# Optimization experiments

Hardware: AMD Instinct MI355X
Metric: run time of the kernel (lower is better)

The kernel has to match this reference:

```python
import jax, jax.numpy as jnp
import numpy as np

# Config (matches init_kwargs)
B, N, F, S, T, L = 4, 128, 128, 5, 32, 2
R_MAX = 10.0
AVG_NEI = 16.0
# ell index of each of the 16 spherical-harmonic components (l=0..3)
ELL_IDX = np.array([0] + [1]*3 + [2]*5 + [3]*7)


def _edges(n):
    # fully-connected directed edge list without self loops (static)
    i = np.arange(n)
    s = np.repeat(i, n)
    r = np.tile(i, n)
    m = s != r
    return jnp.asarray(s[m]), jnp.asarray(r[m])


def _sh(u):
    # real spherical harmonics up to ell=3, component normalization, unit input
    x, y, z = u[..., 0], u[..., 1], u[..., 2]
    s3, s5, s15 = 3**0.5, 5**0.5, 15**0.5
    s35_8, s105, s21_8, s7 = (35/8)**0.5, 105**0.5, (21/8)**0.5, 7**0.5
    comps = [jnp.ones_like(x),
             s3*x, s3*y, s3*z,
             s15*x*y, s15*y*z, 0.5*s5*(3*z*z - 1), s15*x*z, 0.5*s15*(x*x - y*y),
             s35_8*y*(3*x*x - y*y), s105*x*y*z, s21_8*y*(5*z*z - 1),
             0.5*s7*z*(5*z*z - 3), s21_8*x*(5*z*z - 1),
             0.5*s105*z*(x*x - y*y), s35_8*x*(x*x - 3*y*y)]
    return jnp.stack(comps, axis=-1)  # (E,16)


def _forward(positions, node_features, global_features, W_embed, b_embed,
             Wr1, br1, Wr2, Wnode, c1, c2, c3, Wmix0, Wmix1, Wg1, Wg2, Wvout):
    n = positions.shape[1]
    senders, receivers = _edges(n)
    ell = jnp.asarray(ELL_IDX)

    def single(pos, nf, te):
        pos0 = pos
        node_attrs = jax.nn.one_hot(nf - 1, S, dtype=pos.dtype)
        h = jnp.concatenate([node_attrs, jnp.tile(te, (n, 1))], axis=-1)
        scal = h @ W_embed + b_embed            # (N,F) scalar node feats
        vec = jnp.zeros((n, F, 3), pos.dtype)   # (N,F,3) vector node feats
        v = pos[receivers] - pos[senders]       # (E,3)
        lng = jnp.sqrt(jnp.sum(v*v, -1, keepdims=True) + 1e-12)  # (E,1)
        env = 0.5*(jnp.cos(jnp.pi*lng/R_MAX) + 1.0)*(lng < R_MAX)  # cutoff from lengths_0
        for i in range(L):
            u = v / lng
            Y = _sh(u)                                            # (E,16)
            Rw = jax.nn.silu(lng @ Wr1[i] + br1[i]) @ Wr2[i]      # radial MLP (E,4F)
            Rw = (Rw * env).reshape(-1, 4, F)                     # (E,4,F)
            z = (scal @ Wnode[i])[senders]                        # (E,F)
            vdot = jnp.einsum('ecd,ed->ec', vec[senders], u)      # (E,F)
            f = z + vdot
            # tensor-product messages (E,16,F)
            M = Rw[:, ell, :] * Y[:, :, None] * f[:, None, :]
            A = jnp.zeros((n, 16, F), pos.dtype).at[receivers].add(M) / AVG_NEI
            # correlation-3 symmetric-contraction gate via per-ell invariants
            nrm = jnp.zeros((n, 4, F), pos.dtype).at[:, ell, :].add(A*A)
            g = 1.0 + c1[i]*nrm + c2[i]*nrm*nrm + c3[i]*nrm*nrm*nrm
            A = A * g[:, ell, :]
            # linear mix to hidden irreps 128x0e + 128x1o
            scal = A[:, 0, :] @ Wmix0[i]                          # (N,F)
            vec = jnp.einsum('nmc,ck->nkm', A[:, 1:4, :], Wmix1[i])  # (N,F,3)
            # nonlinear readout -> equivariant position update
            gate = jax.nn.silu(scal @ Wg1[i]) @ Wg2[i]            # (N,F)
            mbv = jnp.sum(vec * (gate * Wvout[i])[:, :, None], 1) # (N,3)
            pos = pos + mbv
            v = pos[receivers] - pos[senders]
            lng = jnp.sqrt(jnp.sum(v*v, -1, keepdims=True) + 1e-12)
        return pos - pos0  # predicted noise on positions

    return jax.vmap(single)(positions, node_features, global_features)


def setup_inputs() -> dict:
    key = jax.random.key(0)
    ks = jax.random.split(key, 20)
    sc = 0.1
    p = {}
    p['positions'] = jax.random.normal(ks[0], (B, N, 3), jnp.float32)
    p['node_features'] = jax.random.randint(ks[1], (B, N), 1, S + 1).astype(jnp.int32)
    p['global_features'] = jax.random.normal(ks[2], (B, T), jnp.float32)
    p['W_embed'] = jax.random.normal(ks[3], (S + T, F)) * sc
    p['b_embed'] = jnp.zeros((F,))
    p['Wr1'] = jax.random.normal(ks[4], (L, 1, 64)) * sc
    p['br1'] = jnp.zeros((L, 64))
    p['Wr2'] = jax.random.normal(ks[5], (L, 64, 4 * F)) * sc
    p['Wnode'] = jax.random.normal(ks[6], (L, F, F)) * sc
    p['c1'] = jax.random.normal(ks[7], (L, 4, F)) * 0.01
    p['c2'] = jax.random.normal(ks[8], (L, 4, F)) * 0.001
    p['c3'] = jax.random.normal(ks[9], (L, 4, F)) * 0.0001
    p['Wmix0'] = jax.random.normal(ks[10], (L, F, F)) * sc
    p['Wmix1'] = jax.random.normal(ks[11], (L, F, F)) * sc
    p['Wg1'] = jax.random.normal(ks[12], (L, F, 16)) * sc
    p['Wg2'] = jax.random.normal(ks[13], (L, 16, F)) * sc
    p['Wvout'] = jax.random.normal(ks[14], (L, F)) * sc
    return p


def reference(positions, node_features, global_features, W_embed, b_embed,
              Wr1, br1, Wr2, Wnode, c1, c2, c3, Wmix0, Wmix1, Wg1, Wg2, Wvout):
    return _forward(positions, node_features, global_features, W_embed, b_embed,
                    Wr1, br1, Wr2, Wnode, c1, c2, c3, Wmix0, Wmix1, Wg1, Wg2, Wvout)
```

## Files before the change

kernel.cpp:

```cpp
#include <hip/hip_runtime.h>
#include <hip/hip_bf16.h>
#include <math.h>

#define NB 4
#define NN 128
#define NF 128
#define NS 5
#define NT 32
#define NL 2

typedef __hip_bfloat16 bf16;
typedef short bf16x8 __attribute__((ext_vector_type(8)));
typedef float f32x4 __attribute__((ext_vector_type(4)));

__device__ __forceinline__ float b2f(const bf16 x) { return __bfloat162float(x); }
__device__ __forceinline__ float fast_rcp(float x) { return __builtin_amdgcn_rcpf(x); }
__device__ __forceinline__ float fast_rsq(float x) { return __builtin_amdgcn_rsqf(x); }
__device__ __forceinline__ float silu_fast(float x) { return x * fast_rcp(1.0f + __expf(-x)); }
__device__ __forceinline__ float ldf(const void* p, int i, int fl) {
  return fl ? b2f(((const bf16*)p)[i]) : ((const float*)p)[i];
}
__device__ __forceinline__ short f2bf(float x) {
  unsigned u = __float_as_uint(x);
  unsigned r = (u + 0x7fffu + ((u >> 16) & 1u)) >> 16;
  return (short)r;
}

#define PI_F 3.14159265358979323846f
#define SQRT3_F 1.7320508075688772f

#define POS_OFF 0
#define GF_OFF  1536
#define WE_OFF  1664
#define BE_OFF  6400
#define WR1_OFF 6528
#define BR1_OFF 6656
#define WR2_OFF 6784
#define WN_OFF  72320
#define C1_OFF  105088
#define C2_OFF  106112
#define C3_OFF  107136
#define M0_OFF  108160
#define M1_OFF  140928
#define G1_OFF  173696
#define G2_OFF  177792
#define WV_OFF  181888
#define CVT_TOTAL 182144

__global__ void prep_convert_kernel(
    const void* __restrict__ pos_raw, const int* __restrict__ nfeat,
    const void* __restrict__ gf,  const void* __restrict__ we,
    const void* __restrict__ be,  const void* __restrict__ wr1,
    const void* __restrict__ br1, const void* __restrict__ wr2,
    const void* __restrict__ wn,  const void* __restrict__ c1,
    const void* __restrict__ c2,  const void* __restrict__ c3,
    const void* __restrict__ m0,  const void* __restrict__ m1,
    const void* __restrict__ g1,  const void* __restrict__ g2,
    const void* __restrict__ wv,
    int* __restrict__ flag, float* __restrict__ cvt,
    float* __restrict__ pos_cur, float* __restrict__ z,
    float* __restrict__ vec, float* __restrict__ env,
    float* __restrict__ Ag, short* __restrict__ pkw)
{
  __shared__ float posB[NN*3];
  __shared__ float scs[NF];
  __shared__ int sbad;
  const int tid = threadIdx.x;
  const int bn  = blockIdx.x;
  const int b   = bn >> 7;
  const int n   = bn & 127;

  if (tid == 0) sbad = 0;
  __syncthreads();
  {
    const bf16* p = (const bf16*)pos_raw;
    int bad = 0;
    for (int i = tid; i < NB*NN*3; i += 256) {
      float v = b2f(p[i]);
      if (!(fabsf(v) <= 1024.0f)) bad = 1;
    }
    if (bad) sbad = 1;
  }
  __syncthreads();
  const int fl = sbad ? 0 : 1;
  if (bn == 0 && tid == 0) *flag = fl;

  for (int i = bn*256 + tid; i < CVT_TOTAL; i += 512*256) {
    const void* src; int j;
    if      (i < GF_OFF)  { src = pos_raw; j = i - POS_OFF; }
    else if (i < WE_OFF)  { src = gf;  j = i - GF_OFF; }
    else if (i < BE_OFF)  { src = we;  j = i - WE_OFF; }
    else if (i < WR1_OFF) { src = be;  j = i - BE_OFF; }
    else if (i < BR1_OFF) { src = wr1; j = i - WR1_OFF; }
    else if (i < WR2_OFF) { src = br1; j = i - BR1_OFF; }
    else if (i < WN_OFF)  { src = wr2; j = i - WR2_OFF; }
    else if (i < C1_OFF)  { src = wn;  j = i - WN_OFF; }
    else if (i < C2_OFF)  { src = c1;  j = i - C1_OFF; }
    else if (i < C3_OFF)  { src = c2;  j = i - C2_OFF; }
    else if (i < M0_OFF)  { src = c3;  j = i - C3_OFF; }
    else if (i < M1_OFF)  { src = m0;  j = i - M0_OFF; }
    else if (i < G1_OFF)  { src = m1;  j = i - M1_OFF; }
    else if (i < G2_OFF)  { src = g1;  j = i - G1_OFF; }
    else if (i < WV_OFF)  { src = g2;  j = i - G2_OFF; }
    else                  { src = wv;  j = i - WV_OFF; }
    cvt[i] = fl ? b2f(((const bf16*)src)[j]) : ((const float*)src)[j];
  }

  if (bn < 16) {
    int gid  = bn*256 + tid;
    int lyr  = gid >> 11;
    int r    = gid & 2047;
    int wv   = r >> 9;
    int t    = (r >> 7) & 3;
    int ks   = (r >> 6) & 1;
    int lane = r & 63;
    int qq = lane >> 4, nn = lane & 15;
    int col = wv*64 + t*16 + nn;
    short* dst = pkw + (size_t)gid*8;
    #pragma unroll
    for (int j = 0; j < 8; ++j) {
      int k = ks*32 + qq*8 + j;
      float v = ldf(wr2, lyr*64*512 + k*512 + col, fl);
      if (wv >= 2) v *= SQRT3_F;
      dst[j] = f2bf(v);
    }
  }

  for (int i = tid; i < NN*3; i += 256)
    posB[i] = ldf(pos_raw, b*NN*3 + i, fl);
  if (tid < 128) {
    int sp = nfeat[bn] - 1;
    float acc = ldf(we, sp*NF + tid, fl) + ldf(be, tid, fl);
    #pragma unroll 8
    for (int t = 0; t < NT; ++t)
      acc += ldf(gf, b*NT + t, fl) * ldf(we, (NS + t)*NF + tid, fl);
    scs[tid] = acc;
  }
  __syncthreads();

  if (tid < 128) {
    const int f = tid;
    {
      float px = posB[n*3+0], py = posB[n*3+1], pz = posB[n*3+2];
      float vx = px - posB[f*3+0];
      float vy = py - posB[f*3+1];
      float vz = pz - posB[f*3+2];
      float lng = sqrtf(vx*vx + vy*vy + vz*vz + 1e-12f);
      env[bn*NN + f] = (lng < 10.0f) ? 0.5f*(cosf(PI_F*lng*0.1f) + 1.0f) : 0.0f;
    }
    {
      float acc = 0.f;
      if (fl) {
        const bf16* W = (const bf16*)wn;
        #pragma unroll 8
        for (int k = 0; k < NF; ++k) acc += scs[k] * b2f(W[k*NF + f]);
      } else {
        const float* W = (const float*)wn;
        #pragma unroll 8
        for (int k = 0; k < NF; ++k) acc += scs[k] * W[k*NF + f];
      }
      z[bn*NF + f] = acc;
    }
    vec[((size_t)bn*3 + 0)*NF + f] = 0.f;
    vec[((size_t)bn*3 + 1)*NF + f] = 0.f;
    vec[((size_t)bn*3 + 2)*NF + f] = 0.f;
    float* Arow = Ag + (size_t)bn*4*NF;
    #pragma unroll
    for (int c = 0; c < 4; ++c) Arow[c*NF + f] = 0.f;
    if (f < 3) pos_cur[bn*3 + f] = posB[n*3 + f];
  }
}

__global__ __launch_bounds__(256, 2)
void edge_kernel(const float* __restrict__ pos_cur,
                 const float* __restrict__ z,
                 const float* __restrict__ vec,
                 const float* __restrict__ env,
                 const float* __restrict__ cvt,
                 const short* __restrict__ pk,
                 int layer, float* __restrict__ Ag)
{
  __shared__ float posL[NN*3];
  __shared__ float envL[4][32];
  __shared__ float w1L[64], b1L[64];
  __shared__ __align__(16) short hidA[2][16][72];
  __shared__ __align__(16) float4 zvp[2][4][NF];
  __shared__ __align__(16) float4 uenvL[2][4][4];

  const int tid  = threadIdx.x;
  const int bidx = blockIdx.x;
  const int b    = bidx >> 7;
  const int rt   = (bidx >> 2) & 31;
  const int sg   = bidx & 3;
  const int r0   = rt * 4;
  const int sbase= sg * 32;

  const int wvid  = tid >> 6;
  const int lane  = tid & 63;
  const int n16   = lane & 15;
  const int q     = lane >> 4;
  const int halfB = wvid >> 1;

  for (int i = tid; i < NN*3; i += 256)
    posL[i] = pos_cur[b*NN*3 + i];
  if (tid < 128) {
    int rr = tid >> 5, j = tid & 31;
    envL[rr][j] = env[(b*NN + r0 + rr)*NN + sbase + j];
  }
  if (tid < 64) {
    w1L[tid] = cvt[WR1_OFF + layer*64 + tid];
    b1L[tid] = cvt[BR1_OFF + layer*64 + tid];
  }
  bf16x8 bfr[4][2];
  {
    const bf16x8* PK = (const bf16x8*)pk + (size_t)layer*2048 + wvid*512 + lane;
    #pragma unroll
    for (int t = 0; t < 4; ++t) {
      #pragma unroll
      for (int ks = 0; ks < 2; ++ks)
        bfr[t][ks] = PK[(t*2 + ks)*64];
    }
  }
  float acR[12];
  #pragma unroll
  for (int i = 0; i < 12; ++i) acR[i] = 0.f;

  __syncthreads();

  const int rme = wvid;
  const int hme = lane;
  const float hrx = posL[(r0 + rme)*3 + 0];
  const float hry = posL[(r0 + rme)*3 + 1];
  const float hrz = posL[(r0 + rme)*3 + 2];
  const float w1v = w1L[hme], b1v = b1L[hme];

  const int fS  = tid & 127;
  const int si0 = tid >> 7;

  float4 pv[2];

  #pragma unroll
  for (int rep = 0; rep < 2; ++rep) {
    int gs = b*NN + sbase + 0 + si0 + 2*rep;
    pv[rep].x = z[gs*NF + fS];
    pv[rep].y = vec[((size_t)gs*3 + 0)*NF + fS];
    pv[rep].z = vec[((size_t)gs*3 + 1)*NF + fS];
    pv[rep].w = vec[((size_t)gs*3 + 2)*NF + fS];
  }
  #pragma unroll
  for (int si = 0; si < 4; ++si) {
    int s = sbase + si;
    float vx = hrx - posL[s*3 + 0];
    float vy = hry - posL[s*3 + 1];
    float vz = hrz - posL[s*3 + 2];
    float d = vx*vx + vy*vy + vz*vz + 1e-12f;
    float lng = d * fast_rsq(d);
    hidA[0][rme*4 + si][hme] = f2bf(silu_fast(lng * w1v + b1v));
  }
  if (tid < 16) {
    int r = tid >> 2, si = tid & 3;
    int s = sbase + si;
    float vx = posL[(r0 + r)*3 + 0] - posL[s*3 + 0];
    float vy = posL[(r0 + r)*3 + 1] - posL[s*3 + 1];
    float vz = posL[(r0 + r)*3 + 2] - posL[s*3 + 2];
    float d = vx*vx + vy*vy + vz*vz + 1e-12f;
    float inv = fast_rsq(d);
    float envw = (s == r0 + r) ? 0.f : envL[r][si] * 0.0625f;
    uenvL[0][r][si] = make_float4(vx*inv, vy*inv, vz*inv, envw);
  }
  #pragma unroll
  for (int rep = 0; rep < 2; ++rep)
    zvp[0][si0 + 2*rep][fS] = pv[rep];
  __syncthreads();

  #pragma unroll
  for (int c = 0; c < 8; ++c) {
    const int cb = c & 1, nb = cb ^ 1;
    const int nc0 = (c + 1) * 4;

    if (c < 7) {
      #pragma unroll
      for (int rep = 0; rep < 2; ++rep) {
        int gs = b*NN + sbase + nc0 + si0 + 2*rep;
        pv[rep].x = z[gs*NF + fS];
        pv[rep].y = vec[((size_t)gs*3 + 0)*NF + fS];
        pv[rep].z = vec[((size_t)gs*3 + 1)*NF + fS];
        pv[rep].w = vec[((size_t)gs*3 + 2)*NF + fS];
      }
    }

    bf16x8 af0 = *(const bf16x8*)&hidA[cb][n16][q*8];
    bf16x8 af1 = *(const bf16x8*)&hidA[cb][n16][q*8 + 32];
    float4 ue[4];
    #pragma unroll
    for (int si = 0; si < 4; ++si) ue[si] = uenvL[cb][q][si];

    #pragma unroll
    for (int t = 0; t < 4; ++t) {
      f32x4 Cf = {0.f, 0.f, 0.f, 0.f};
      Cf = __builtin_amdgcn_mfma_f32_16x16x32_bf16(af0, bfr[t][0], Cf, 0, 0, 0);
      Cf = __builtin_amdgcn_mfma_f32_16x16x32_bf16(af1, bfr[t][1], Cf, 0, 0, 0);
      int f = (wvid*64 + t*16 + n16) & 127;
      if (!halfB) {
        float a0 = 0.f;
        #pragma unroll
        for (int si = 0; si < 4; ++si) {
          float4 zv = zvp[cb][si][f];
          float fv = zv.x + ue[si].x*zv.y + ue[si].y*zv.z + ue[si].z*zv.w;
          a0 += (Cf[si] * ue[si].w) * fv;
        }
        acR[t] += a0;
      } else {
        float t1 = 0.f, t2 = 0.f, t3 = 0.f;
        #pragma unroll
        for (int si = 0; si < 4; ++si) {
          float4 zv = zvp[cb][si][f];
          float fv = zv.x + ue[si].x*zv.y + ue[si].y*zv.z + ue[si].z*zv.w;
          float tt = (Cf[si] * ue[si].w) * fv;
          t1 += tt * ue[si].x;
          t2 += tt * ue[si].y;
          t3 += tt * ue[si].z;
        }
        acR[t*3 + 0] += t1;
        acR[t*3 + 1] += t2;
        acR[t*3 + 2] += t3;
      }
    }

    if (c < 7) {
      #pragma unroll
      for (int si = 0; si < 4; ++si) {
        int s = sbase + nc0 + si;
        float vx = hrx - posL[s*3 + 0];
        float vy = hry - posL[s*3 + 1];
        float vz = hrz - posL[s*3 + 2];
        float d = vx*vx + vy*vy + vz*vz + 1e-12f;
        float lng = d * fast_rsq(d);
        hidA[nb][rme*4 + si][hme] = f2bf(silu_fast(lng * w1v + b1v));
      }
      if (tid < 16) {
        int r = tid >> 2, si = tid & 3;
        int s = sbase + nc0 + si;
        float vx = posL[(r0 + r)*3 + 0] - posL[s*3 + 0];
        float vy = posL[(r0 + r)*3 + 1] - posL[s*3 + 1];
        float vz = posL[(r0 + r)*3 + 2] - posL[s*3 + 2];
        float d = vx*vx + vy*vy + vz*vz + 1e-12f;
        float inv = fast_rsq(d);
        float envw = (s == r0 + r) ? 0.f : envL[r][nc0 + si] * 0.0625f;
        uenvL[nb][r][si] = make_float4(vx*inv, vy*inv, vz*inv, envw);
      }
      #pragma unroll
      for (int rep = 0; rep < 2; ++rep)
        zvp[nb][si0 + 2*rep][fS] = pv[rep];
    }
    __syncthreads();
  }

  const size_t rowbase = (size_t)(b*NN + r0 + q)*4;
  if (!halfB) {
    #pragma unroll
    for (int t = 0; t < 4; ++t) {
      int f = (wvid*64 + t*16 + n16) & 127;
      atomicAdd(Ag + (rowbase + 0)*NF + f, acR[t]);
    }
  } else {
    #pragma unroll
    for (int t = 0; t < 4; ++t) {
      int f = (wvid*64 + t*16 + n16) & 127;
      atomicAdd(Ag + (rowbase + 1)*NF + f, acR[t*3 + 0]);
      atomicAdd(Ag + (rowbase + 2)*NF + f, acR[t*3 + 1]);
      atomicAdd(Ag + (rowbase + 3)*NF + f, acR[t*3 + 2]);
    }
  }
}

__global__ __launch_bounds__(256)
void node_kernel(float* __restrict__ Ag,
                 const float* __restrict__ cvt,
                 int layer, int last,
                 float* __restrict__ vec,
                 float* __restrict__ z,
                 float* __restrict__ pos_cur,
                 const int* __restrict__ flag,
                 void* __restrict__ out)
{
  const int bn  = blockIdx.x;
  const int tid = threadIdx.x;
  const int f   = tid & 127;
  __shared__ float Ash[4][NF];
  __shared__ float scs[NF];
  __shared__ float h16[16];
  __shared__ float red[2][4];
  __shared__ float P[8][32][17];
  __shared__ float Pg[8][16];

  if (tid < 128) {
    float* Arow = Ag + (size_t)bn*4*NF;
    float a0 = Arow[0*NF + f];
    float a1 = Arow[1*NF + f];
    float a2 = Arow[2*NF + f];
    float a3 = Arow[3*NF + f];
    Arow[0*NF + f] = 0.f;
    Arow[1*NF + f] = 0.f;
    Arow[2*NF + f] = 0.f;
    Arow[3*NF + f] = 0.f;
    float n0 = a0*a0;
    float C1 = cvt[C1_OFF + (layer*4 + 0)*NF + f];
    float C2 = cvt[C2_OFF + (layer*4 + 0)*NF + f];
    float C3 = cvt[C3_OFF + (layer*4 + 0)*NF + f];
    float g0 = 1.0f + C1*n0 + C2*n0*n0 + C3*n0*n0*n0;
    float n1 = a1*a1 + a2*a2 + a3*a3;
    float D1 = cvt[C1_OFF + (layer*4 + 1)*NF + f];
    float D2 = cvt[C2_OFF + (layer*4 + 1)*NF + f];
    float D3 = cvt[C3_OFF + (layer*4 + 1)*NF + f];
    float g1 = 1.0f + D1*n1 + D2*n1*n1 + D3*n1*n1*n1;
    Ash[0][f] = a0 * g0;
    Ash[1][f] = a1 * g1;
    Ash[2][f] = a2 * g1;
    Ash[3][f] = a3 * g1;
  }
  __syncthreads();

  {
    const float* M0 = cvt + M0_OFF + layer*NF*NF;
    const float* M1 = cvt + M1_OFF + layer*NF*NF;
    const int kh = tid >> 5;
    const int fq = tid & 31;
    float s0=0.f,s1=0.f,s2=0.f,s3=0.f;
    float w00=0.f,w01=0.f,w02=0.f,w03=0.f;
    float w10=0.f,w11=0.f,w12=0.f,w13=0.f;
    float w20=0.f,w21=0.f,w22=0.f,w23=0.f;
    #pragma unroll 4
    for (int kk = 0; kk < 16; ++kk) {
      int k = kh*16 + kk;
      float a0 = Ash[0][k], a1 = Ash[1][k], a2 = Ash[2][k], a3 = Ash[3][k];
      float4 m0 = *(const float4*)(M0 + k*NF + fq*4);
      float4 m1 = *(const float4*)(M1 + k*NF + fq*4);
      s0 += a0*m0.x; s1 += a0*m0.y; s2 += a0*m0.z; s3 += a0*m0.w;
      w00 += a1*m1.x; w01 += a1*m1.y; w02 += a1*m1.z; w03 += a1*m1.w;
      w10 += a2*m1.x; w11 += a2*m1.y; w12 += a2*m1.z; w13 += a2*m1.w;
      w20 += a3*m1.x; w21 += a3*m1.y; w22 += a3*m1.z; w23 += a3*m1.w;
    }
    float* Pp = &P[kh][fq][0];
    Pp[0]=s0;  Pp[1]=s1;  Pp[2]=s2;  Pp[3]=s3;
    Pp[4]=w00; Pp[5]=w01; Pp[6]=w02; Pp[7]=w03;
    Pp[8]=w10; Pp[9]=w11; Pp[10]=w12; Pp[11]=w13;
    Pp[12]=w20; Pp[13]=w21; Pp[14]=w22; Pp[15]=w23;
  }
  __syncthreads();

  float v0 = 0.f, v1 = 0.f, v2 = 0.f;
  if (tid < 128) {
    int fq = f >> 2, j = f & 3;
    float sn = 0.f;
    #pragma unroll
    for (int kh = 0; kh < 8; ++kh) {
      const float* Pp = &P[kh][fq][0];
      sn += Pp[j];
      v0 += Pp[4 + j];
      v1 += Pp[8 + j];
      v2 += Pp[12 + j];
    }
    scs[f] = sn;
  }
  __syncthreads();

  if (!last) {
    const float* W = cvt + WN_OFF + (layer+1)*NF*NF;
    const int kh = tid >> 5;
    const int fq = tid & 31;
    float s0=0.f,s1=0.f,s2=0.f,s3=0.f;
    #pragma unroll 4
    for (int kk = 0; kk < 16; ++kk) {
      int k = kh*16 + kk;
      float a = scs[k];
      float4 m = *(const float4*)(W + k*NF + fq*4);
      s0 += a*m.x; s1 += a*m.y; s2 += a*m.z; s3 += a*m.w;
    }
    float* Pp = &P[kh][fq][0];
    Pp[0]=s0; Pp[1]=s1; Pp[2]=s2; Pp[3]=s3;
  }
  if (tid < 128) {
    const float* G1 = cvt + G1_OFF + layer*NF*16;
    int o = tid & 15, g = tid >> 4;
    float acc = 0.f;
    #pragma unroll
    for (int kk = 0; kk < 16; ++kk) {
      int k = g*16 + kk;
      acc += scs[k] * G1[k*16 + o];
    }
    Pg[g][o] = acc;
  }
  __syncthreads();

  if (!last && tid < 128) {
    int fq = f >> 2, j = f & 3;
    float acc = 0.f;
    #pragma unroll
    for (int kh = 0; kh < 8; ++kh) acc += P[kh][fq][j];
    z[bn*NF + f] = acc;
  }
  if (tid < 16) {
    float acc = 0.f;
    #pragma unroll
    for (int g = 0; g < 8; ++g) acc += Pg[g][tid];
    h16[tid] = silu_fast(acc);
  }
  __syncthreads();

  if (tid < 128) {
    const float* G2 = cvt + G2_OFF + layer*16*NF;
    float gate = 0.f;
    #pragma unroll
    for (int j = 0; j < 16; ++j)
      gate += h16[j] * G2[j*NF + f];
    float gv = gate * cvt[WV_OFF + layer*NF + f];

    vec[((size_t)bn*3 + 0)*NF + f] = v0;
    vec[((size_t)bn*3 + 1)*NF + f] = v1;
    vec[((size_t)bn*3 + 2)*NF + f] = v2;

    float p0 = v0*gv, p1 = v1*gv, p2 = v2*gv;
    #pragma unroll
    for (int off = 32; off > 0; off >>= 1) {
      p0 += __shfl_down(p0, off, 64);
      p1 += __shfl_down(p1, off, 64);
      p2 += __shfl_down(p2, off, 64);
    }
    int wave = f >> 6;
    if ((f & 63) == 0) { red[wave][0] = p0; red[wave][1] = p1; red[wave][2] = p2; }
  }
  __syncthreads();
  if (tid == 0) {
    float m0 = red[0][0] + red[1][0];
    float m1 = red[0][1] + red[1][1];
    float m2 = red[0][2] + red[1][2];
    float px = pos_cur[bn*3+0] + m0;
    float py = pos_cur[bn*3+1] + m1;
    float pz = pos_cur[bn*3+2] + m2;
    pos_cur[bn*3+0] = px;
    pos_cur[bn*3+1] = py;
    pos_cur[bn*3+2] = pz;
    if (last) {
      float ox = px - cvt[POS_OFF + bn*3+0];
      float oy = py - cvt[POS_OFF + bn*3+1];
      float oz = pz - cvt[POS_OFF + bn*3+2];
      if (*flag) {
        bf16* o = (bf16*)out;
        o[bn*3+0] = __float2bfloat16(ox);
        o[bn*3+1] = __float2bfloat16(oy);
        o[bn*3+2] = __float2bfloat16(oz);
      } else {
        float* o = (float*)out;
        o[bn*3+0] = ox;
        o[bn*3+1] = oy;
        o[bn*3+2] = oz;
      }
    }
  }
}

extern "C" void kernel_launch(void* const* d_in, const int* in_sizes, int n_in,
                              void* d_out, int out_size, void* d_ws, size_t ws_size,
                              hipStream_t stream)
{
  (void)in_sizes; (void)n_in; (void)out_size; (void)ws_size;
  const int* nfeat = (const int*)d_in[1];

  float* ws      = (float*)d_ws;
  int*   flag    = (int*)ws;
  float* cvt     = ws + 16;
  float* pos_cur = cvt + CVT_TOTAL;
  float* z       = pos_cur + NB*NN*3;
  float* vec     = z + NB*NN*NF;
  float* Ag      = vec + NB*NN*3*NF;
  float* env     = Ag + NB*NN*4*NF;
  short* pk      = (short*)(env + NB*NN*NN);

  prep_convert_kernel<<<512, 256, 0, stream>>>(
      d_in[0], nfeat, d_in[2], d_in[3], d_in[4], d_in[5], d_in[6], d_in[7],
      d_in[8], d_in[9], d_in[10], d_in[11], d_in[12], d_in[13], d_in[14],
      d_in[15], d_in[16], flag, cvt, pos_cur, z, vec, env, Ag, pk);
  for (int i = 0; i < NL; ++i) {
    edge_kernel<<<512, 256, 0, stream>>>(pos_cur, z, vec, env, cvt, pk, i, Ag);
    node_kernel<<<NB*NN, 256, 0, stream>>>(Ag, cvt, i, (i == NL-1) ? 1 : 0,
                                           vec, z, pos_cur, flag, d_out);
  }
}
```

Baseline: 144.8 us.

## Fuse edge and node kernels into one per-receiver block with ping-pong buffers

Each block now owns one receiver node and loops over all 128 senders, so the aggregated messages are reduced in registers and shared memory instead of through global atomics. The node update then runs in the same block, which removes the separate node kernel, the Ag buffer and its zeroing. Positions, z and vec are double-buffered across the two layers, and layer 0 skips loading the all-zero vec. The cost is a larger per-block loop with no sender split across blocks, more registers for the 8-entry prefetch, and a shared-memory union. A few branch reorderings in the weight-conversion routine look odd and could be fragile.

```diff
diff --git a/kernel.cpp b/kernel.cpp
--- a/kernel.cpp
+++ b/kernel.cpp
@@ -59,8 +59,7 @@
     const void* __restrict__ wv,
     int* __restrict__ flag, float* __restrict__ cvt,
     float* __restrict__ pos_cur, float* __restrict__ z,
-    float* __restrict__ vec, float* __restrict__ env,
-    float* __restrict__ Ag, short* __restrict__ pkw)
+    float* __restrict__ env, short* __restrict__ pkw)
 {
   __shared__ float posB[NN*3];
   __shared__ float scs[NF];
@@ -92,9 +91,8 @@
     else if (i < BE_OFF)  { src = we;  j = i - WE_OFF; }
     else if (i < WR1_OFF) { src = be;  j = i - BE_OFF; }
     else if (i < BR1_OFF) { src = wr1; j = i - WR1_OFF; }
-    else if (i < WR2_OFF) { src = br1; j = i - BR1_OFF; }
-    else if (i < WN_OFF)  { src = wr2; j = i - WR2_OFF; }
-    else if (i < C1_OFF)  { src = wn;  j = i - WN_OFF; }
+    else if (i < WN_OFF)  { src = br1; j = i - BR1_OFF; }
+    else if (i < C1_OFF)  { src = wr2; j = i - WR2_OFF; }
     else if (i < C2_OFF)  { src = c1;  j = i - C1_OFF; }
     else if (i < C3_OFF)  { src = c2;  j = i - C2_OFF; }
     else if (i < M0_OFF)  { src = c3;  j = i - C3_OFF; }
@@ -103,6 +101,8 @@
     else if (i < G2_OFF)  { src = g1;  j = i - G1_OFF; }
     else if (i < WV_OFF)  { src = g2;  j = i - G2_OFF; }
     else                  { src = wv;  j = i - WV_OFF; }
+    if (i < WN_OFF && i >= C1_OFF) { }
+    if      (i >= WN_OFF && i < C1_OFF) { src = wn; j = i - WN_OFF; }
     cvt[i] = fl ? b2f(((const bf16*)src)[j]) : ((const float*)src)[j];
   }
 
@@ -110,18 +110,18 @@
     int gid  = bn*256 + tid;
     int lyr  = gid >> 11;
     int r    = gid & 2047;
-    int wv   = r >> 9;
+    int wv2  = r >> 9;
     int t    = (r >> 7) & 3;
     int ks   = (r >> 6) & 1;
     int lane = r & 63;
     int qq = lane >> 4, nn = lane & 15;
-    int col = wv*64 + t*16 + nn;
+    int col = wv2*64 + t*16 + nn;
     short* dst = pkw + (size_t)gid*8;
     #pragma unroll
     for (int j = 0; j < 8; ++j) {
       int k = ks*32 + qq*8 + j;
       float v = ldf(wr2, lyr*64*512 + k*512 + col, fl);
-      if (wv >= 2) v *= SQRT3_F;
+      if (wv2 >= 2) v *= SQRT3_F;
       dst[j] = f2bf(v);
     }
   }
@@ -161,39 +161,40 @@
       }
       z[bn*NF + f] = acc;
     }
-    vec[((size_t)bn*3 + 0)*NF + f] = 0.f;
-    vec[((size_t)bn*3 + 1)*NF + f] = 0.f;
-    vec[((size_t)bn*3 + 2)*NF + f] = 0.f;
-    float* Arow = Ag + (size_t)bn*4*NF;
-    #pragma unroll
-    for (int c = 0; c < 4; ++c) Arow[c*NF + f] = 0.f;
     if (f < 3) pos_cur[bn*3 + f] = posB[n*3 + f];
   }
 }
 
 __global__ __launch_bounds__(256, 2)
-void edge_kernel(const float* __restrict__ pos_cur,
-                 const float* __restrict__ z,
-                 const float* __restrict__ vec,
-                 const float* __restrict__ env,
-                 const float* __restrict__ cvt,
-                 const short* __restrict__ pk,
-                 int layer, float* __restrict__ Ag)
+void fused_kernel(const float* __restrict__ posIn, float* __restrict__ posOut,
+                  const float* __restrict__ zIn,  float* __restrict__ zOut,
+                  const float* __restrict__ vecIn, float* __restrict__ vecOut,
+                  const float* __restrict__ env,  const float* __restrict__ cvt,
+                  const short* __restrict__ pk, int layer, int last,
+                  const int* __restrict__ flag, void* __restrict__ out)
 {
+  union SM {
+    float4 zvp[2][16][NF];
+    struct {
+      float P[8][32][17];
+      float Pg[8][16];
+      float scs[NF];
+      float h16[16];
+      float red[2][4];
+    } nd;
+  };
+  __shared__ __align__(16) SM sm;
   __shared__ float posL[NN*3];
-  __shared__ float envL[4][32];
+  __shared__ float envL[NN];
   __shared__ float w1L[64], b1L[64];
   __shared__ __align__(16) short hidA[2][16][72];
-  __shared__ __align__(16) float4 zvp[2][4][NF];
-  __shared__ __align__(16) float4 uenvL[2][4][4];
+  __shared__ __align__(16) float4 uenvL[2][16];
+  __shared__ float Ash[4][NF];
 
   const int tid  = threadIdx.x;
   const int bidx = blockIdx.x;
   const int b    = bidx >> 7;
-  const int rt   = (bidx >> 2) & 31;
-  const int sg   = bidx & 3;
-  const int r0   = rt * 4;
-  const int sbase= sg * 32;
+  const int n    = bidx & 127;
 
   const int wvid  = tid >> 6;
   const int lane  = tid & 63;
@@ -202,11 +203,8 @@
   const int halfB = wvid >> 1;
 
   for (int i = tid; i < NN*3; i += 256)
-    posL[i] = pos_cur[b*NN*3 + i];
-  if (tid < 128) {
-    int rr = tid >> 5, j = tid & 31;
-    envL[rr][j] = env[(b*NN + r0 + rr)*NN + sbase + j];
-  }
+    posL[i] = posIn[b*NN*3 + i];
+  if (tid < 128) envL[tid] = env[(size_t)(b*NN + n)*NN + tid];
   if (tid < 64) {
     w1L[tid] = cvt[WR1_OFF + layer*64 + tid];
     b1L[tid] = cvt[BR1_OFF + layer*64 + tid];
@@ -227,65 +225,68 @@
 
   __syncthreads();
 
-  const int rme = wvid;
-  const int hme = lane;
-  const float hrx = posL[(r0 + rme)*3 + 0];
-  const float hry = posL[(r0 + rme)*3 + 1];
-  const float hrz = posL[(r0 + rme)*3 + 2];
-  const float w1v = w1L[hme], b1v = b1L[hme];
+  const float hrx = posL[n*3 + 0];
+  const float hry = posL[n*3 + 1];
+  const float hrz = posL[n*3 + 2];
+  const float w1v = w1L[lane], b1v = b1L[lane];
 
   const int fS  = tid & 127;
   const int si0 = tid >> 7;
 
-  float4 pv[2];
+  float4 pv[8];
 
   #pragma unroll
-  for (int rep = 0; rep < 2; ++rep) {
-    int gs = b*NN + sbase + 0 + si0 + 2*rep;
-    pv[rep].x = z[gs*NF + fS];
-    pv[rep].y = vec[((size_t)gs*3 + 0)*NF + fS];
-    pv[rep].z = vec[((size_t)gs*3 + 1)*NF + fS];
-    pv[rep].w = vec[((size_t)gs*3 + 2)*NF + fS];
+  for (int rep = 0; rep < 8; ++rep) {
+    int sl = si0 + 2*rep;
+    int gs = b*NN + sl;
+    pv[rep].x = zIn[gs*NF + fS];
+    if (layer) {
+      pv[rep].y = vecIn[((size_t)gs*3 + 0)*NF + fS];
+      pv[rep].z = vecIn[((size_t)gs*3 + 1)*NF + fS];
+      pv[rep].w = vecIn[((size_t)gs*3 + 2)*NF + fS];
+    } else { pv[rep].y = 0.f; pv[rep].z = 0.f; pv[rep].w = 0.f; }
   }
   #pragma unroll
-  for (int si = 0; si < 4; ++si) {
-    int s = sbase + si;
+  for (int j = 0; j < 4; ++j) {
+    int si = wvid*4 + j;
+    int s  = si;
     float vx = hrx - posL[s*3 + 0];
     float vy = hry - posL[s*3 + 1];
     float vz = hrz - posL[s*3 + 2];
     float d = vx*vx + vy*vy + vz*vz + 1e-12f;
     float lng = d * fast_rsq(d);
-    hidA[0][rme*4 + si][hme] = f2bf(silu_fast(lng * w1v + b1v));
+    hidA[0][si][lane] = f2bf(silu_fast(lng * w1v + b1v));
   }
   if (tid < 16) {
-    int r = tid >> 2, si = tid & 3;
-    int s = sbase + si;
-    float vx = posL[(r0 + r)*3 + 0] - posL[s*3 + 0];
-    float vy = posL[(r0 + r)*3 + 1] - posL[s*3 + 1];
-    float vz = posL[(r0 + r)*3 + 2] - posL[s*3 + 2];
+    int s = tid;
+    float vx = hrx - posL[s*3 + 0];
+    float vy = hry - posL[s*3 + 1];
+    float vz = hrz - posL[s*3 + 2];
     float d = vx*vx + vy*vy + vz*vz + 1e-12f;
     float inv = fast_rsq(d);
-    float envw = (s == r0 + r) ? 0.f : envL[r][si] * 0.0625f;
-    uenvL[0][r][si] = make_float4(vx*inv, vy*inv, vz*inv, envw);
+    float envw = (s == n) ? 0.f : envL[s] * 0.0625f;
+    uenvL[0][tid] = make_float4(vx*inv, vy*inv, vz*inv, envw);
   }
   #pragma unroll
-  for (int rep = 0; rep < 2; ++rep)
-    zvp[0][si0 + 2*rep][fS] = pv[rep];
-  __syncthreads();
-
-  #pragma unroll
+  for (int rep = 0; rep < 8; ++rep)
+    sm.zvp[0][si0 + 2*rep][fS] = pv[rep];
+  __syncthreads();
+
+  #pragma unroll 2
   for (int c = 0; c < 8; ++c) {
     const int cb = c & 1, nb = cb ^ 1;
-    const int nc0 = (c + 1) * 4;
+    const int nc0 = (c + 1) * 16;
 
     if (c < 7) {
       #pragma unroll
-      for (int rep = 0; rep < 2; ++rep) {
-        int gs = b*NN + sbase + nc0 + si0 + 2*rep;
-        pv[rep].x = z[gs*NF + fS];
-        pv[rep].y = vec[((size_t)gs*3 + 0)*NF + fS];
-        pv[rep].z = vec[((size_t)gs*3 + 1)*NF + fS];
-        pv[rep].w = vec[((size_t)gs*3 + 2)*NF + fS];
+      for (int rep = 0; rep < 8; ++rep) {
+        int gs = b*NN + nc0 + si0 + 2*rep;
+        pv[rep].x = zIn[gs*NF + fS];
+        if (layer) {
+          pv[rep].y = vecIn[((size_t)gs*3 + 0)*NF + fS];
+          pv[rep].z = vecIn[((size_t)gs*3 + 1)*NF + fS];
+          pv[rep].w = vecIn[((size_t)gs*3 + 2)*NF + fS];
+        } else { pv[rep].y = 0.f; pv[rep].z = 0.f; pv[rep].w = 0.f; }
       }
     }
 
@@ -293,7 +294,7 @@
     bf16x8 af1 = *(const bf16x8*)&hidA[cb][n16][q*8 + 32];
     float4 ue[4];
     #pragma unroll
-    for (int si = 0; si < 4; ++si) ue[si] = uenvL[cb][q][si];
+    for (int r = 0; r < 4; ++r) ue[r] = uenvL[cb][q*4 + r];
 
     #pragma unroll
     for (int t = 0; t < 4; ++t) {
@@ -304,22 +305,22 @@
       if (!halfB) {
         float a0 = 0.f;
         #pragma unroll
-        for (int si = 0; si < 4; ++si) {
-          float4 zv = zvp[cb][si][f];
-          float fv = zv.x + ue[si].x*zv.y + ue[si].y*zv.z + ue[si].z*zv.w;
-          a0 += (Cf[si] * ue[si].w) * fv;
+        for (int r = 0; r < 4; ++r) {
+          float4 zv = sm.zvp[cb][q*4 + r][f];
+          float fv = zv.x + ue[r].x*zv.y + ue[r].y*zv.z + ue[r].z*zv.w;
+          a0 += (Cf[r] * ue[r].w) * fv;
         }
         acR[t] += a0;
       } else {
         float t1 = 0.f, t2 = 0.f, t3 = 0.f;
         #pragma unroll
-        for (int si = 0; si < 4; ++si) {
-          float4 zv = zvp[cb][si][f];
-          float fv = zv.x + ue[si].x*zv.y + ue[si].y*zv.z + ue[si].z*zv.w;
-          float tt = (Cf[si] * ue[si].w) * fv;
-          t1 += tt * ue[si].x;
-          t2 += tt * ue[si].y;
-          t3 += tt * ue[si].z;
+        for (int r = 0; r < 4; ++r) {
+          float4 zv = sm.zvp[cb][q*4 + r][f];
+          float fv = zv.x + ue[r].x*zv.y + ue[r].y*zv.z + ue[r].z*zv.w;
+          float tt = (Cf[r] * ue[r].w) * fv;
+          t1 += tt * ue[r].x;
+          t2 += tt * ue[r].y;
+          t3 += tt * ue[r].z;
         }
         acR[t*3 + 0] += t1;
         acR[t*3 + 1] += t2;
@@ -329,95 +330,77 @@
 
     if (c < 7) {
       #pragma unroll
-      for (int si = 0; si < 4; ++si) {
-        int s = sbase + nc0 + si;
+      for (int j = 0; j < 4; ++j) {
+        int si = wvid*4 + j;
+        int s  = nc0 + si;
         float vx = hrx - posL[s*3 + 0];
         float vy = hry - posL[s*3 + 1];
         float vz = hrz - posL[s*3 + 2];
         float d = vx*vx + vy*vy + vz*vz + 1e-12f;
         float lng = d * fast_rsq(d);
-        hidA[nb][rme*4 + si][hme] = f2bf(silu_fast(lng * w1v + b1v));
+        hidA[nb][si][lane] = f2bf(silu_fast(lng * w1v + b1v));
       }
       if (tid < 16) {
-        int r = tid >> 2, si = tid & 3;
-        int s = sbase + nc0 + si;
-        float vx = posL[(r0 + r)*3 + 0] - posL[s*3 + 0];
-        float vy = posL[(r0 + r)*3 + 1] - posL[s*3 + 1];
-        float vz = posL[(r0 + r)*3 + 2] - posL[s*3 + 2];
+        int s = nc0 + tid;
+        float vx = hrx - posL[s*3 + 0];
+        float vy = hry - posL[s*3 + 1];
+        float vz = hrz - posL[s*3 + 2];
         float d = vx*vx + vy*vy + vz*vz + 1e-12f;
         float inv = fast_rsq(d);
-        float envw = (s == r0 + r) ? 0.f : envL[r][nc0 + si] * 0.0625f;
-        uenvL[nb][r][si] = make_float4(vx*inv, vy*inv, vz*inv, envw);
+        float envw = (s == n) ? 0.f : envL[s] * 0.0625f;
+        uenvL[nb][tid] = make_float4(vx*inv, vy*inv, vz*inv, envw);
       }
       #pragma unroll
-      for (int rep = 0; rep < 2; ++rep)
-        zvp[nb][si0 + 2*rep][fS] = pv[rep];
+      for (int rep = 0; rep < 8; ++rep)
+        sm.zvp[nb][si0 + 2*rep][fS] = pv[rep];
     }
     __syncthreads();
   }
 
-  const size_t rowbase = (size_t)(b*NN + r0 + q)*4;
-  if (!halfB) {
+  #pragma unroll
+  for (int i = 0; i < 12; ++i) {
+    float v = acR[i];
+    v += __shfl_xor(v, 16, 64);
+    v += __shfl_xor(v, 32, 64);
+    acR[i] = v;
+  }
+  if (lane < 16) {
     #pragma unroll
     for (int t = 0; t < 4; ++t) {
-      int f = (wvid*64 + t*16 + n16) & 127;
-      atomicAdd(Ag + (rowbase + 0)*NF + f, acR[t]);
-    }
-  } else {
-    #pragma unroll
-    for (int t = 0; t < 4; ++t) {
-      int f = (wvid*64 + t*16 + n16) & 127;
-      atomicAdd(Ag + (rowbase + 1)*NF + f, acR[t*3 + 0]);
-      atomicAdd(Ag + (rowbase + 2)*NF + f, acR[t*3 + 1]);
-      atomicAdd(Ag + (rowbase + 3)*NF + f, acR[t*3 + 2]);
-    }
-  }
-}
-
-__global__ __launch_bounds__(256)
-void node_kernel(float* __restrict__ Ag,
-                 const float* __restrict__ cvt,
-                 int layer, int last,
-                 float* __restrict__ vec,
-                 float* __restrict__ z,
-                 float* __restrict__ pos_cur,
-                 const int* __restrict__ flag,
-                 void* __restrict__ out)
-{
-  const int bn  = blockIdx.x;
-  const int tid = threadIdx.x;
-  const int f   = tid & 127;
-  __shared__ float Ash[4][NF];
-  __shared__ float scs[NF];
-  __shared__ float h16[16];
-  __shared__ float red[2][4];
-  __shared__ float P[8][32][17];
-  __shared__ float Pg[8][16];
+      int f = (wvid*64 + t*16 + lane) & 127;
+      if (!halfB) {
+        Ash[0][f] = acR[t];
+      } else {
+        Ash[1][f] = acR[t*3 + 0];
+        Ash[2][f] = acR[t*3 + 1];
+        Ash[3][f] = acR[t*3 + 2];
+      }
+    }
+  }
+  __syncthreads();
+
+  const int fn = tid & 127;
+  float v0 = 0.f, v1 = 0.f, v2 = 0.f;
 
   if (tid < 128) {
-    float* Arow = Ag + (size_t)bn*4*NF;
-    float a0 = Arow[0*NF + f];
-    float a1 = Arow[1*NF + f];
-    float a2 = Arow[2*NF + f];
-    float a3 = Arow[3*NF + f];
-    Arow[0*NF + f] = 0.f;
-    Arow[1*NF + f] = 0.f;
-    Arow[2*NF + f] = 0.f;
-    Arow[3*NF + f] = 0.f;
+    float a0 = Ash[0][fn];
+    float a1 = Ash[1][fn];
+    float a2 = Ash[2][fn];
+    float a3 = Ash[3][fn];
     float n0 = a0*a0;
-    float C1 = cvt[C1_OFF + (layer*4 + 0)*NF + f];
-    float C2 = cvt[C2_OFF + (layer*4 + 0)*NF + f];
-    float C3 = cvt[C3_OFF + (layer*4 + 0)*NF + f];
+    float C1 = cvt[C1_OFF + (layer*4 + 0)*NF + fn];
+    float C2 = cvt[C2_OFF + (layer*4 + 0)*NF + fn];
+    float C3 = cvt[C3_OFF + (layer*4 + 0)*NF + fn];
     float g0 = 1.0f + C1*n0 + C2*n0*n0 + C3*n0*n0*n0;
     float n1 = a1*a1 + a2*a2 + a3*a3;
-    float D1 = cvt[C1_OFF + (layer*4 + 1)*NF + f];
-    float D2 = cvt[C2_OFF + (layer*4 + 1)*NF + f];
-    float D3 = cvt[C3_OFF + (layer*4 + 1)*NF + f];
+    float D1 = cvt[C1_OFF + (layer*4 + 1)*NF + fn];
+    float D2 = cvt[C2_OFF + (layer*4 + 1)*NF + fn];
+    float D3 = cvt[C3_OFF + (layer*4 + 1)*NF + fn];
     float g1 = 1.0f + D1*n1 + D2*n1*n1 + D3*n1*n1*n1;
-    Ash[0][f] = a0 * g0;
-    Ash[1][f] = a1 * g1;
-    Ash[2][f] = a2 * g1;
-    Ash[3][f] = a3 * g1;
+    Ash[0][fn] = a0 * g0;
+    Ash[1][fn] = a1 * g1;
+    Ash[2][fn] = a2 * g1;
+    Ash[3][fn] = a3 * g1;
   }
   __syncthreads();
 
@@ -441,7 +424,7 @@
       w10 += a2*m1.x; w11 += a2*m1.y; w12 += a2*m1.z; w13 += a2*m1.w;
       w20 += a3*m1.x; w21 += a3*m1.y; w22 += a3*m1.z; w23 += a3*m1.w;
     }
-    float* Pp = &P[kh][fq][0];
+    float* Pp = &sm.nd.P[kh][fq][0];
     Pp[0]=s0;  Pp[1]=s1;  Pp[2]=s2;  Pp[3]=s3;
     Pp[4]=w00; Pp[5]=w01; Pp[6]=w02; Pp[7]=w03;
     Pp[8]=w10; Pp[9]=w11; Pp[10]=w12; Pp[11]=w13;
@@ -449,19 +432,18 @@
   }
   __syncthreads();
 
-  float v0 = 0.f, v1 = 0.f, v2 = 0.f;
   if (tid < 128) {
-    int fq = f >> 2, j = f & 3;
+    int fq = fn >> 2, j = fn & 3;
     float sn = 0.f;
     #pragma unroll
     for (int kh = 0; kh < 8; ++kh) {
-      const float* Pp = &P[kh][fq][0];
+      const float* Pp = &sm.nd.P[kh][fq][0];
       sn += Pp[j];
       v0 += Pp[4 + j];
       v1 += Pp[8 + j];
       v2 += Pp[12 + j];
     }
-    scs[f] = sn;
+    sm.nd.scs[fn] = sn;
   }
   __syncthreads();
 
@@ -473,11 +455,11 @@
     #pragma unroll 4
     for (int kk = 0; kk < 16; ++kk) {
       int k = kh*16 + kk;
-      float a = scs[k];
+      float a = sm.nd.scs[k];
       float4 m = *(const float4*)(W + k*NF + fq*4);
       s0 += a*m.x; s1 += a*m.y; s2 += a*m.z; s3 += a*m.w;
     }
-    float* Pp = &P[kh][fq][0];
+    float* Pp = &sm.nd.P[kh][fq][0];
     Pp[0]=s0; Pp[1]=s1; Pp[2]=s2; Pp[3]=s3;
   }
   if (tid < 128) {
@@ -487,24 +469,24 @@
     #pragma unroll
     for (int kk = 0; kk < 16; ++kk) {
       int k = g*16 + kk;
-      acc += scs[k] * G1[k*16 + o];
-    }
-    Pg[g][o] = acc;
+      acc += sm.nd.scs[k] * G1[k*16 + o];
+    }
+    sm.nd.Pg[g][o] = acc;
   }
   __syncthreads();
 
   if (!last && tid < 128) {
-    int fq = f >> 2, j = f & 3;
+    int fq = fn >> 2, j = fn & 3;
     float acc = 0.f;
     #pragma unroll
-    for (int kh = 0; kh < 8; ++kh) acc += P[kh][fq][j];
-    z[bn*NF + f] = acc;
+    for (int kh = 0; kh < 8; ++kh) acc += sm.nd.P[kh][fq][j];
+    zOut[bidx*NF + fn] = acc;
   }
   if (tid < 16) {
     float acc = 0.f;
     #pragma unroll
-    for (int g = 0; g < 8; ++g) acc += Pg[g][tid];
-    h16[tid] = silu_fast(acc);
+    for (int g = 0; g < 8; ++g) acc += sm.nd.Pg[g][tid];
+    sm.nd.h16[tid] = silu_fast(acc);
   }
   __syncthreads();
 
@@ -513,12 +495,14 @@
     float gate = 0.f;
     #pragma unroll
     for (int j = 0; j < 16; ++j)
-      gate += h16[j] * G2[j*NF + f];
-    float gv = gate * cvt[WV_OFF + layer*NF + f];
-
-    vec[((size_t)bn*3 + 0)*NF + f] = v0;
-    vec[((size_t)bn*3 + 1)*NF + f] = v1;
-    vec[((size_t)bn*3 + 2)*NF + f] = v2;
+      gate += sm.nd.h16[j] * G2[j*NF + fn];
+    float gv = gate * cvt[WV_OFF + layer*NF + fn];
+
+    if (!last) {
+      vecOut[((size_t)bidx*3 + 0)*NF + fn] = v0;
+      vecOut[((size_t)bidx*3 + 1)*NF + fn] = v1;
+      vecOut[((size_t)bidx*3 + 2)*NF + fn] = v2;
+    }
 
     float p0 = v0*gv, p1 = v1*gv, p2 = v2*gv;
     #pragma unroll
@@ -527,34 +511,39 @@
       p1 += __shfl_down(p1, off, 64);
       p2 += __shfl_down(p2, off, 64);
     }
-    int wave = f >> 6;
-    if ((f & 63) == 0) { red[wave][0] = p0; red[wave][1] = p1; red[wave][2] = p2; }
+    int wave = fn >> 6;
+    if ((fn & 63) == 0) {
+      sm.nd.red[wave][0] = p0;
+      sm.nd.red[wave][1] = p1;
+      sm.nd.red[wave][2] = p2;
+    }
   }
   __syncthreads();
   if (tid == 0) {
-    float m0 = red[0][0] + red[1][0];
-    float m1 = red[0][1] + red[1][1];
-    float m2 = red[0][2] + red[1][2];
-    float px = pos_cur[bn*3+0] + m0;
-    float py = pos_cur[bn*3+1] + m1;
-    float pz = pos_cur[bn*3+2] + m2;
-    pos_cur[bn*3+0] = px;
-    pos_cur[bn*3+1] = py;
-    pos_cur[bn*3+2] = pz;
-    if (last) {
-      float ox = px - cvt[POS_OFF + bn*3+0];
-      float oy = py - cvt[POS_OFF + bn*3+1];
-      float oz = pz - cvt[POS_OFF + bn*3+2];
+    float m0 = sm.nd.red[0][0] + sm.nd.red[1][0];
+    float m1 = sm.nd.red[0][1] + sm.nd.red[1][1];
+    float m2 = sm.nd.red[0][2] + sm.nd.red[1][2];
+    float px = posL[n*3+0] + m0;
+    float py = posL[n*3+1] + m1;
+    float pz = posL[n*3+2] + m2;
+    if (!last) {
+      posOut[bidx*3+0] = px;
+      posOut[bidx*3+1] = py;
+      posOut[bidx*3+2] = pz;
+    } else {
+      float ox = px - cvt[POS_OFF + bidx*3+0];
+      float oy = py - cvt[POS_OFF + bidx*3+1];
+      float oz = pz - cvt[POS_OFF + bidx*3+2];
       if (*flag) {
         bf16* o = (bf16*)out;
-        o[bn*3+0] = __float2bfloat16(ox);
-        o[bn*3+1] = __float2bfloat16(oy);
-        o[bn*3+2] = __float2bfloat16(oz);
+        o[bidx*3+0] = __float2bfloat16(ox);
+        o[bidx*3+1] = __float2bfloat16(oy);
+        o[bidx*3+2] = __float2bfloat16(oz);
       } else {
         float* o = (float*)out;
-        o[bn*3+0] = ox;
-        o[bn*3+1] = oy;
-        o[bn*3+2] = oz;
+        o[bidx*3+0] = ox;
+        o[bidx*3+1] = oy;
+        o[bidx*3+2] = oz;
       }
     }
   }
@@ -567,23 +556,24 @@
   (void)in_sizes; (void)n_in; (void)out_size; (void)ws_size;
   const int* nfeat = (const int*)d_in[1];
 
-  float* ws      = (float*)d_ws;
-  int*   flag    = (int*)ws;
-  float* cvt     = ws + 16;
-  float* pos_cur = cvt + CVT_TOTAL;
-  float* z       = pos_cur + NB*NN*3;
-  float* vec     = z + NB*NN*NF;
-  float* Ag      = vec + NB*NN*3*NF;
-  float* env     = Ag + NB*NN*4*NF;
-  short* pk      = (short*)(env + NB*NN*NN);
+  float* ws   = (float*)d_ws;
+  int*   flag = (int*)ws;
+  float* cvt  = ws + 16;
+  float* pos0 = cvt + CVT_TOTAL;
+  float* pos1 = pos0 + NB*NN*3;
+  float* z0   = pos1 + NB*NN*3;
+  float* z1   = z0 + NB*NN*NF;
+  float* vec1 = z1 + NB*NN*NF;
+  float* env  = vec1 + NB*NN*3*NF;
+  short* pk   = (short*)(env + NB*NN*NN);
 
   prep_convert_kernel<<<512, 256, 0, stream>>>(
       d_in[0], nfeat, d_in[2], d_in[3], d_in[4], d_in[5], d_in[6], d_in[7],
       d_in[8], d_in[9], d_in[10], d_in[11], d_in[12], d_in[13], d_in[14],
-      d_in[15], d_in[16], flag, cvt, pos_cur, z, vec, env, Ag, pk);
-  for (int i = 0; i < NL; ++i) {
-    edge_kernel<<<512, 256, 0, stream>>>(pos_cur, z, vec, env, cvt, pk, i, Ag);
-    node_kernel<<<NB*NN, 256, 0, stream>>>(Ag, cvt, i, (i == NL-1) ? 1 : 0,
-                                           vec, z, pos_cur, flag, d_out);
-  }
+      d_in[15], d_in[16], flag, cvt, pos0, z0, env, pk);
+
+  fused_kernel<<<512, 256, 0, stream>>>(pos0, pos1, z0, z1, (const float*)0,
+                                        vec1, env, cvt, pk, 0, 0, flag, d_out);
+  fused_kernel<<<512, 256, 0, stream>>>(pos1, (float*)0, z1, (float*)0, vec1,
+                                        (float*)0, env, cvt, pk, 1, 1, flag, d_out);
 }
```

Measured after the change: 145.9 us. No clear change (+0.8%).
